# Kernel optimization log

Measured on AMD Instinct MI355X. Metric: run time of the kernel, lower is better.

The kernel has to match this reference:

```python
import math
import jax, jax.numpy as jnp
import numpy as np

H, PQ, PV = 12, 8, 12
C_S = 384
INF, EPS = 1e5, 1e-8
SOFTPLUS_INV_1 = 0.541324854612918


def _rand_rot(key, shape):
    """Random rotation matrices via normalized quaternions, shape + (3,3)."""
    q = jax.random.normal(key, shape + (4,))
    q = q / jnp.linalg.norm(q, axis=-1, keepdims=True)
    w, x, y, z = q[..., 0], q[..., 1], q[..., 2], q[..., 3]
    R = jnp.stack([
        1 - 2 * (y * y + z * z), 2 * (x * y - w * z), 2 * (x * z + w * y),
        2 * (x * y + w * z), 1 - 2 * (x * x + z * z), 2 * (y * z - w * x),
        2 * (x * z - w * y), 2 * (y * z + w * x), 1 - 2 * (x * x + y * y),
    ], axis=-1).reshape(shape + (3, 3))
    return R


def setup_inputs() -> dict:
    key = jax.random.key(0)
    ks = jax.random.split(key, 12)
    B, N1, N2 = 2, 2048, 512
    s1 = jax.random.normal(ks[0], (B, N1, C_S), dtype=jnp.float32)
    s2 = jax.random.normal(ks[1], (B, N2, C_S), dtype=jnp.float32)
    r1_rot = _rand_rot(ks[2], (B, N1)).astype(jnp.float32)
    r2_rot = _rand_rot(ks[3], (B, N2)).astype(jnp.float32)
    r1_trans = jax.random.normal(ks[4], (B, N1, 3), dtype=jnp.float32)
    r2_trans = jax.random.normal(ks[5], (B, N2, 3), dtype=jnp.float32)
    mask1 = jnp.ones((B, N1), dtype=jnp.float32)
    mask2 = jnp.ones((B, N2), dtype=jnp.float32)
    Wq = jax.random.normal(ks[6], (C_S, H * PQ * 3), dtype=jnp.float32) / math.sqrt(C_S)
    Wkv = jax.random.normal(ks[7], (C_S, H * (PQ + PV) * 3), dtype=jnp.float32) / math.sqrt(C_S)
    head_weights = jnp.full((H,), SOFTPLUS_INV_1, dtype=jnp.float32)
    Wout = jax.random.normal(ks[8], (H * PV * 4, C_S), dtype=jnp.float32) * 0.02
    bout = jnp.zeros((C_S,), dtype=jnp.float32)
    return {"s1": s1, "s2": s2, "r1_rot": r1_rot, "r1_trans": r1_trans,
            "r2_rot": r2_rot, "r2_trans": r2_trans, "mask1": mask1, "mask2": mask2,
            "Wq": Wq, "Wkv": Wkv, "head_weights": head_weights,
            "Wout": Wout, "bout": bout}


def reference(s1, s2, r1_rot, r1_trans, r2_rot, r2_trans, mask1, mask2,
              Wq, Wkv, head_weights, Wout, bout):
    B, N1, _ = s1.shape
    N2 = s2.shape[1]

    # query points: linear -> [B,N1,3,H,PQ] (torch split/stack layout) -> local [B,N1,H,PQ,3]
    q = jnp.moveaxis((s1 @ Wq).reshape(B, N1, 3, H, PQ), 2, -1)
    # rigid apply: R x + t (global frame)
    q = jnp.einsum('bimn,bihpn->bihpm', r1_rot, q) + r1_trans[:, :, None, None, :]

    kv = jnp.moveaxis((s2 @ Wkv).reshape(B, N2, 3, H, PQ + PV), 2, -1)
    kv = jnp.einsum('bjmn,bjhpn->bjhpm', r2_rot, kv) + r2_trans[:, :, None, None, :]
    k, v = kv[..., :PQ, :], kv[..., PQ:, :]  # [B,N2,H,PQ,3], [B,N2,H,PV,3]

    # sum_p ||q_p - k_p||^2 via norm expansion (avoids [B,N1,N2,H,PQ,3] tensor)
    qn = jnp.sum(q * q, axis=(-1, -2))                     # [B,N1,H]
    kn = jnp.sum(k * k, axis=(-1, -2))                     # [B,N2,H]
    cross = jnp.einsum('bihpc,bjhpc->bijh', q, k)          # [B,N1,N2,H]
    d2 = qn[:, :, None, :] + kn[:, None, :, :] - 2.0 * cross

    hw = jax.nn.softplus(head_weights) * math.sqrt(1.0 / (3 * (PQ * 9.0 / 2)))
    att = jnp.transpose(-0.5 * d2 * hw, (0, 3, 1, 2))      # [B,H,N1,N2]
    bias = INF * (mask1[:, :, None] * mask2[:, None, :] - 1.0)
    a = jax.nn.softmax(att + bias[:, None], axis=-1)

    o = jnp.einsum('bhij,bjhpc->bihpc', a, v)              # [B,N1,H,PV,3]
    # rigid invert_apply: R^T (x - t), back into local frame of residue i
    o_loc = jnp.einsum('bimn,bihpm->bihpn', r1_rot, o - r1_trans[:, :, None, None, :])

    dists = jnp.sqrt(jnp.sum(o_loc * o_loc, axis=-1) + EPS)   # [B,N1,H,PV]
    o_flat = o_loc.reshape(B, N1, H * PV, 3)
    feats = jnp.concatenate([o_flat[..., 0], o_flat[..., 1], o_flat[..., 2],
                             dists.reshape(B, N1, H * PV)], axis=-1)
    return feats @ Wout + bout
```

## Files before the change

kernel.cpp:

```cpp
#include <hip/hip_runtime.h>
#include <math.h>

#define B_ 2
#define N1_ 2048
#define N2_ 512
#define CS_ 384
#define H_ 12
#define PQ_ 8
#define PV_ 12
#define PKV_ 20
#define CQ_ (H_*PQ_*3)
#define CKV_ (H_*PKV_*3)
#define INF_ 100000.0f
#define HW_SCALE_ 0.09622504486493764f
#define LOG2E_ 1.4426950408889634f

typedef __attribute__((ext_vector_type(8))) short bf16x8;
typedef __attribute__((ext_vector_type(4))) float f32x4;

__device__ inline unsigned short f2bf(float x) {
  unsigned u = __float_as_uint(x);
  u += 0x7fffu + ((u >> 16) & 1u);
  return (unsigned short)(u >> 16);
}

__device__ inline bf16x8 cvt8(const float* __restrict__ p) {
  float4 a = *(const float4*)p;
  float4 b = *(const float4*)(p + 4);
  bf16x8 r;
  r[0] = (short)f2bf(a.x); r[1] = (short)f2bf(a.y);
  r[2] = (short)f2bf(a.z); r[3] = (short)f2bf(a.w);
  r[4] = (short)f2bf(b.x); r[5] = (short)f2bf(b.y);
  r[6] = (short)f2bf(b.z); r[7] = (short)f2bf(b.w);
  return r;
}

#define TQ_   108
#define TKV_  276
#define TWO_  216
#define VPAD_ 72
#define KN_   12
#define S1B_  768
#define S2B_  192
#define PREP_GRID_ (TQ_+TKV_+TWO_+VPAD_+KN_+S1B_+S2B_)
__global__ __launch_bounds__(256) void prep_kernel(
    const float* __restrict__ Wq, const float* __restrict__ Wkv,
    const float* __restrict__ Wout,
    const float* __restrict__ s1, const float* __restrict__ s2,
    unsigned short* __restrict__ wqT, unsigned short* __restrict__ wkvT,
    unsigned short* __restrict__ woutT,
    unsigned short* __restrict__ vtb, float* __restrict__ kn,
    unsigned short* __restrict__ s1b, unsigned short* __restrict__ s2b)
{
  __shared__ float lds[32][33];
  int blk = blockIdx.x, t = threadIdx.x;
  int rr0 = t >> 5, cc = t & 31;

  const float* src = nullptr; unsigned short* dst = nullptr;
  int K = 0, N = 0, k0 = 0, n0 = 0;
  if (blk < TQ_) {
    src = Wq; dst = wqT; K = 384; N = CQ_;
    k0 = (blk % 12) * 32; n0 = (blk / 12) * 32;
  } else if (blk < TQ_ + TKV_) {
    int b2 = blk - TQ_;
    src = Wkv; dst = wkvT; K = 384; N = CKV_;
    k0 = (b2 % 12) * 32; n0 = (b2 / 12) * 32;
  } else if (blk < TQ_ + TKV_ + TWO_) {
    int b3 = blk - TQ_ - TKV_;
    src = Wout; dst = woutT; K = 576; N = CS_;
    k0 = (b3 % 18) * 32; n0 = (b3 / 18) * 32;
  } else if (blk < TQ_ + TKV_ + TWO_ + VPAD_) {
    int idx = (blk - TQ_ - TKV_ - TWO_)*256 + t;
    int f = idx * 8;
    int run = f >> 9, off = f & 511;
    int bh = run / 12, cc2 = 36 + run % 12;
    uint4 z = {0u,0u,0u,0u};
    *(uint4*)(vtb + ((size_t)bh*48 + cc2)*512 + off) = z;
    return;
  } else if (blk < TQ_ + TKV_ + TWO_ + VPAD_ + KN_) {
    int idx = (blk - TQ_ - TKV_ - TWO_ - VPAD_)*256 + t;
    float4 z = {0.f,0.f,0.f,0.f};
    *(float4*)(kn + (size_t)idx*4) = z;
    return;
  } else if (blk < TQ_ + TKV_ + TWO_ + VPAD_ + KN_ + S1B_) {
    size_t idx = (size_t)(blk - TQ_ - TKV_ - TWO_ - VPAD_ - KN_)*256 + t;
    *(bf16x8*)(s1b + idx*8) = cvt8(s1 + idx*8);
    return;
  } else {
    size_t idx = (size_t)(blk - TQ_ - TKV_ - TWO_ - VPAD_ - KN_ - S1B_)*256 + t;
    *(bf16x8*)(s2b + idx*8) = cvt8(s2 + idx*8);
    return;
  }

  #pragma unroll
  for (int rr = 0; rr < 4; ++rr) {
    int r = rr0 + rr*8;
    if (n0 + cc < N) lds[r][cc] = src[(size_t)(k0 + r)*N + n0 + cc];
  }
  __syncthreads();
  #pragma unroll
  for (int rr = 0; rr < 4; ++rr) {
    int r = rr0 + rr*8;
    if (n0 + r < N) dst[(size_t)(n0 + r)*K + k0 + cc] = f2bf(lds[cc][r]);
  }
}

__global__ __launch_bounds__(256) void proj_mfma(
    const unsigned short* __restrict__ s1b, const unsigned short* __restrict__ s2b,
    const unsigned short* __restrict__ wqT, const unsigned short* __restrict__ wkvT,
    const float* __restrict__ r1_rot, const float* __restrict__ r1_trans,
    const float* __restrict__ r2_rot, const float* __restrict__ r2_trans,
    unsigned short* __restrict__ qgb, float* __restrict__ qn,
    unsigned short* __restrict__ kgb, unsigned short* __restrict__ vtb,
    float* __restrict__ kn)
{
  int wave = threadIdx.x >> 6, lane = threadIdx.x & 63;
  int col = lane & 15, g = lane >> 4;

  if (blockIdx.x < 384) {
    int wg = blockIdx.x*4 + wave;
    int strip = wg / 6;
    int nt = wg % 6;
    int i0 = strip * 16;

    f32x4 ax = {0.f,0.f,0.f,0.f}, ay = ax, az = ax;
    const unsigned short* arow = s1b + (size_t)(i0 + col)*CS_;
    const unsigned short* bx = wqT + (size_t)((nt     )*16 + col)*CS_;
    const unsigned short* by = wqT + (size_t)((nt +  6)*16 + col)*CS_;
    const unsigned short* bz = wqT + (size_t)((nt + 12)*16 + col)*CS_;
    #pragma unroll
    for (int k = 0; k < CS_; k += 32) {
      bf16x8 a = *(const bf16x8*)(arow + k + g*8);
      ax = __builtin_amdgcn_mfma_f32_16x16x32_bf16(a, *(const bf16x8*)(bx + k + g*8), ax, 0,0,0);
      ay = __builtin_amdgcn_mfma_f32_16x16x32_bf16(a, *(const bf16x8*)(by + k + g*8), ay, 0,0,0);
      az = __builtin_amdgcn_mfma_f32_16x16x32_bf16(a, *(const bf16x8*)(bz + k + g*8), az, 0,0,0);
    }

    int p = nt*16 + col;
    int h = p >> 3, pq = p & 7;
    float qsum[4];
    #pragma unroll
    for (int r = 0; r < 4; ++r) {
      int row = i0 + g*4 + r;
      const float* R  = r1_rot   + (size_t)row*9;
      const float* tr = r1_trans + (size_t)row*3;
      float x = ax[r], y = ay[r], z = az[r];
      float g0 = R[0]*x + R[1]*y + R[2]*z + tr[0];
      float g1 = R[3]*x + R[4]*y + R[5]*z + tr[1];
      float g2 = R[6]*x + R[7]*y + R[8]*z + tr[2];
      int b = row >> 11, i = row & (N1_-1);
      size_t rbase = ((size_t)(b*H_ + h)*N1_ + i)*32;
      qgb[rbase + pq*3]     = f2bf(g0);
      qgb[rbase + pq*3 + 1] = f2bf(g1);
      qgb[rbase + pq*3 + 2] = f2bf(g2);
      if (pq == 7) {
        uint4 z4 = {0u,0u,0u,0u};
        *(uint4*)(qgb + rbase + 24) = z4;
      }
      qsum[r] = g0*g0 + g1*g1 + g2*g2;
    }
    #pragma unroll
    for (int r = 0; r < 4; ++r) {
      qsum[r] += __shfl_xor(qsum[r], 1);
      qsum[r] += __shfl_xor(qsum[r], 2);
      qsum[r] += __shfl_xor(qsum[r], 4);
    }
    if ((col & 7) == 0) {
      int hh = nt*2 + (col >> 3);
      #pragma unroll
      for (int r = 0; r < 4; ++r) {
        int row = i0 + g*4 + r;
        int b = row >> 11, i = row & (N1_-1);
        qn[(size_t)(b*H_ + hh)*N1_ + i] = qsum[r];
      }
    }
  } else {
    int wg = (blockIdx.x - 384)*4 + wave;
    int strip = wg / 15;
    int nt = wg % 15;
    int row0 = strip * 16;

    f32x4 ax = {0.f,0.f,0.f,0.f}, ay = ax, az = ax;
    const unsigned short* arow = s2b + (size_t)(row0 + col)*CS_;
    const unsigned short* bx = wkvT + (size_t)(nt*16       + col)*CS_;
    const unsigned short* by = wkvT + (size_t)(nt*16 + 240 + col)*CS_;
    const unsigned short* bz = wkvT + (size_t)(nt*16 + 480 + col)*CS_;
    #pragma unroll
    for (int k = 0; k < CS_; k += 32) {
      bf16x8 a = *(const bf16x8*)(arow + k + g*8);
      ax = __builtin_amdgcn_mfma_f32_16x16x32_bf16(a, *(const bf16x8*)(bx + k + g*8), ax, 0,0,0);
      ay = __builtin_amdgcn_mfma_f32_16x16x32_bf16(a, *(const bf16x8*)(by + k + g*8), ay, 0,0,0);
      az = __builtin_amdgcn_mfma_f32_16x16x32_bf16(a, *(const bf16x8*)(bz + k + g*8), az, 0,0,0);
    }

    int p = nt*16 + col;
    int h = p / PKV_, pp = p % PKV_;
    #pragma unroll
    for (int r = 0; r < 4; ++r) {
      int row = row0 + g*4 + r;
      const float* R  = r2_rot   + (size_t)row*9;
      const float* tr = r2_trans + (size_t)row*3;
      float x = ax[r], y = ay[r], z = az[r];
      float g0 = R[0]*x + R[1]*y + R[2]*z + tr[0];
      float g1 = R[3]*x + R[4]*y + R[5]*z + tr[1];
      float g2 = R[6]*x + R[7]*y + R[8]*z + tr[2];
      int b = row >> 9, j = row & (N2_-1);
      int bh = b*H_ + h;
      if (pp < PQ_) {
        size_t base = ((size_t)bh*N2_ + j)*32 + pp*3;
        kgb[base]   = f2bf(g0);
        kgb[base+1] = f2bf(g1);
        kgb[base+2] = f2bf(g2);
        if (pp == 0) {
          uint4 z4 = {0u,0u,0u,0u};
          *(uint4*)(kgb + ((size_t)bh*N2_ + j)*32 + 24) = z4;
        }
        atomicAdd(&kn[(size_t)bh*N2_ + j], g0*g0 + g1*g1 + g2*g2);
      } else {
        int comp = (pp - PQ_)*3;
        size_t base = ((size_t)bh*48 + comp)*512 + j;
        vtb[base]        = f2bf(g0);
        vtb[base + 512]  = f2bf(g1);
        vtb[base + 1024] = f2bf(g2);
      }
    }
  }
}

#define RSTRIDE 72
#define OSTRIDE 51
#define WSLOT 3328
#define FSTRIDE 584
__global__ __launch_bounds__(768) void attn_fused(
    const unsigned short* __restrict__ qgb, const float* __restrict__ qn,
    const unsigned short* __restrict__ kgb, const unsigned short* __restrict__ vtb,
    const float* __restrict__ kn, const float* __restrict__ mask1,
    const float* __restrict__ mask2, const float* __restrict__ hwts,
    const float* __restrict__ rot, const float* __restrict__ trans,
    const unsigned short* __restrict__ woutT, const float* __restrict__ bout,
    float* __restrict__ out)
{
  __shared__ __align__(16) unsigned char ovl[12*WSLOT];
  __shared__ __align__(16) unsigned short feats_s[16][FSTRIDE];
  __shared__ float l_s[12][16];

  int wave = threadIdx.x >> 6;
  int lane = threadIdx.x & 63;
  int col = lane & 15, g = lane >> 4;
  int b = blockIdx.x >> 7;
  int it = blockIdx.x & 127;
  int h = wave;
  int bh = b*H_ + h;

  unsigned short* ps = (unsigned short*)(ovl + wave*WSLOT);
  float*          os = (float*)(ovl + wave*WSLOT);

  float hw   = logf(1.0f + __expf(hwts[h])) * HW_SCALE_;
  float hwl  = hw * LOG2E_;
  float mneg = -INF_ * LOG2E_;

  bf16x8 qa = *(const bf16x8*)(qgb + (((size_t)bh*N1_ + it*16 + col)*32 + g*8));

  float ar[4], m1l[4];
  #pragma unroll
  for (int r = 0; r < 4; ++r) {
    int ig = it*16 + g*4 + r;
    ar[r]  = -0.5f*hwl * qn[(size_t)bh*N1_ + ig];
    m1l[r] = mask1[b*N1_ + ig] * (INF_*LOG2E_);
  }

  f32x4 ot[3];
  #pragma unroll
  for (int m = 0; m < 3; ++m) ot[m] = (f32x4){0.f,0.f,0.f,0.f};
  float l[4] = {0.f,0.f,0.f,0.f};

  const unsigned short* kbase = kgb + (size_t)bh*N2_*32;
  const unsigned short* vbase = vtb + (size_t)bh*48*512;
  const float* knp = kn + (size_t)bh*N2_;
  const float* m2p = mask2 + b*N2_;

  for (int jt = 0; jt < 8; ++jt) {
    int j0 = jt*64;
    #pragma unroll
    for (int nt = 0; nt < 4; ++nt) {
      int jg = j0 + nt*16 + col;
      bf16x8 kb = *(const bf16x8*)(kbase + ((size_t)jg*32 + g*8));
      f32x4 dotv = __builtin_amdgcn_mfma_f32_16x16x32_bf16(
          qa, kb, (f32x4){0.f,0.f,0.f,0.f}, 0, 0, 0);
      float bc  = -0.5f*hwl*knp[jg];
      float m2c = m2p[jg];
      #pragma unroll
      for (int r = 0; r < 4; ++r) {
        float logit = fmaf(hwl, dotv[r], fmaf(m1l[r], m2c, mneg) + (ar[r] + bc));
        float w = __builtin_amdgcn_exp2f(logit);
        l[r] += w;
        ps[(g*4 + r)*RSTRIDE + nt*16 + col] = f2bf(w);
      }
    }
    #pragma unroll
    for (int ks = 0; ks < 2; ++ks) {
      bf16x8 pb = *(const bf16x8*)&ps[col*RSTRIDE + ks*32 + g*8];
      #pragma unroll
      for (int mtv = 0; mtv < 3; ++mtv) {
        bf16x8 va = *(const bf16x8*)(vbase +
            ((size_t)(mtv*16 + col))*512 + j0 + ks*32 + g*8);
        ot[mtv] = __builtin_amdgcn_mfma_f32_16x16x32_bf16(va, pb, ot[mtv], 0, 0, 0);
      }
    }
  }

  #pragma unroll
  for (int r = 0; r < 4; ++r) {
    l[r] += __shfl_xor(l[r], 1);
    l[r] += __shfl_xor(l[r], 2);
    l[r] += __shfl_xor(l[r], 4);
    l[r] += __shfl_xor(l[r], 8);
  }
  __builtin_amdgcn_sched_barrier(0);
  if (col == 0) {
    #pragma unroll
    for (int r = 0; r < 4; ++r) l_s[wave][g*4 + r] = l[r];
  }
  #pragma unroll
  for (int mtv = 0; mtv < 3; ++mtv)
    #pragma unroll
    for (int r = 0; r < 4; ++r)
      os[col*OSTRIDE + mtv*16 + g*4 + r] = ot[mtv][r];
  __syncthreads();

  {
    float inv = 1.0f / l_s[wave][col];
    int ig = it*16 + col;
    int row = b*N1_ + ig;
    const float* R  = rot   + (size_t)row*9;
    const float* tr = trans + (size_t)row*3;
    float R00=R[0],R01=R[1],R02=R[2],R10=R[3],R11=R[4],R12=R[5],R20=R[6],R21=R[7],R22=R[8];
    float t0=tr[0], t1=tr[1], t2=tr[2];
    int h12 = h*PV_;
    #pragma unroll
    for (int p = 0; p < 3; ++p) {
      int pt = g*3 + p;
      float ox = os[col*OSTRIDE + pt*3+0]*inv - t0;
      float oy = os[col*OSTRIDE + pt*3+1]*inv - t1;
      float oz = os[col*OSTRIDE + pt*3+2]*inv - t2;
      float lx = R00*ox + R10*oy + R20*oz;
      float ly = R01*ox + R11*oy + R21*oz;
      float lz = R02*ox + R12*oy + R22*oz;
      float dist = sqrtf(lx*lx + ly*ly + lz*lz + 1e-8f);
      feats_s[col][      h12 + pt] = f2bf(lx);
      feats_s[col][144 + h12 + pt] = f2bf(ly);
      feats_s[col][288 + h12 + pt] = f2bf(lz);
      feats_s[col][432 + h12 + pt] = f2bf(dist);
    }
  }
  __syncthreads();

  {
    int n0 = wave * 32;
    f32x4 acc0 = {0.f,0.f,0.f,0.f}, acc1 = acc0;
    const unsigned short* b0 = woutT + (size_t)(n0      + col)*576;
    const unsigned short* b1 = woutT + (size_t)(n0 + 16 + col)*576;
    #pragma unroll 3
    for (int k = 0; k < 576; k += 32) {
      bf16x8 a = *(const bf16x8*)&feats_s[col][k + g*8];
      acc0 = __builtin_amdgcn_mfma_f32_16x16x32_bf16(a, *(const bf16x8*)(b0 + k + g*8), acc0, 0,0,0);
      acc1 = __builtin_amdgcn_mfma_f32_16x16x32_bf16(a, *(const bf16x8*)(b1 + k + g*8), acc1, 0,0,0);
    }
    int rowbase = b*N1_ + it*16;
    float bb0 = bout[n0 + col];
    float bb1 = bout[n0 + 16 + col];
    #pragma unroll
    for (int r = 0; r < 4; ++r) {
      size_t orow = (size_t)(rowbase + g*4 + r)*CS_;
      out[orow + n0 + col]      = acc0[r] + bb0;
      out[orow + n0 + 16 + col] = acc1[r] + bb1;
    }
  }
}

extern "C" void kernel_launch(void* const* d_in, const int* in_sizes, int n_in,
                              void* d_out, int out_size, void* d_ws, size_t ws_size,
                              hipStream_t stream) {
  const float* s1       = (const float*)d_in[0];
  const float* s2       = (const float*)d_in[1];
  const float* r1_rot   = (const float*)d_in[2];
  const float* r1_trans = (const float*)d_in[3];
  const float* r2_rot   = (const float*)d_in[4];
  const float* r2_trans = (const float*)d_in[5];
  const float* mask1    = (const float*)d_in[6];
  const float* mask2    = (const float*)d_in[7];
  const float* Wq       = (const float*)d_in[8];
  const float* Wkv      = (const float*)d_in[9];
  const float* hwts     = (const float*)d_in[10];
  const float* Wout     = (const float*)d_in[11];
  const float* bout     = (const float*)d_in[12];
  float* out = (float*)d_out;

  float* qn = (float*)d_ws;
  float* kn = qn + (size_t)B_*H_*N1_;
  unsigned short* qgb  = (unsigned short*)(kn + (size_t)B_*H_*N2_);
  unsigned short* kgb  = qgb  + (size_t)B_*H_*N1_*32;
  unsigned short* vtb  = kgb  + (size_t)B_*H_*N2_*32;
  unsigned short* wqT  = vtb  + (size_t)B_*H_*48*512;
  unsigned short* wkvT = wqT  + (size_t)CQ_*CS_;
  unsigned short* woutT= wkvT + (size_t)CKV_*CS_;
  unsigned short* s1b  = woutT+ (size_t)CS_*576;
  unsigned short* s2b  = s1b  + (size_t)B_*N1_*CS_;

  prep_kernel<<<PREP_GRID_, 256, 0, stream>>>(
      Wq, Wkv, Wout, s1, s2, wqT, wkvT, woutT, vtb, kn, s1b, s2b);
  proj_mfma<<<624, 256, 0, stream>>>(s1b, s2b, wqT, wkvT, r1_rot, r1_trans,
                                     r2_rot, r2_trans, qgb, qn, kgb, vtb, kn);
  attn_fused<<<B_*(N1_/16), 768, 0, stream>>>(qgb, qn, kgb, vtb, kn, mask1, mask2,
                                              hwts, r1_rot, r1_trans, woutT, bout, out);
}
```

Baseline: 148.6 us.

## Split attention over key halves and projection K-dim across waves with merges

The attention kernel now launches twice as many blocks, each covering half of the N2 keys. Each block writes its partial output and row sums to a global buffer, and the second block of each pair to finish, detected through an atomic counter, merges both halves and runs the epilogue. The projection kernel splits the K reduction across two waves per output tile and merges the two partial sums through LDS. The aim is more parallelism and better CU occupancy, at the cost of extra global traffic, atomics, fences and a doubled epilogue-free block count.

```diff
diff --git a/kernel.cpp b/kernel.cpp
--- a/kernel.cpp
+++ b/kernel.cpp
@@ -42,7 +42,8 @@
 #define KN_   12
 #define S1B_  768
 #define S2B_  192
-#define PREP_GRID_ (TQ_+TKV_+TWO_+VPAD_+KN_+S1B_+S2B_)
+#define CNTB_ 1
+#define PREP_GRID_ (TQ_+TKV_+TWO_+VPAD_+KN_+S1B_+S2B_+CNTB_)
 __global__ __launch_bounds__(256) void prep_kernel(
     const float* __restrict__ Wq, const float* __restrict__ Wkv,
     const float* __restrict__ Wout,
@@ -50,7 +51,8 @@
     unsigned short* __restrict__ wqT, unsigned short* __restrict__ wkvT,
     unsigned short* __restrict__ woutT,
     unsigned short* __restrict__ vtb, float* __restrict__ kn,
-    unsigned short* __restrict__ s1b, unsigned short* __restrict__ s2b)
+    unsigned short* __restrict__ s1b, unsigned short* __restrict__ s2b,
+    unsigned* __restrict__ cnt)
 {
   __shared__ float lds[32][33];
   int blk = blockIdx.x, t = threadIdx.x;
@@ -86,10 +88,13 @@
     size_t idx = (size_t)(blk - TQ_ - TKV_ - TWO_ - VPAD_ - KN_)*256 + t;
     *(bf16x8*)(s1b + idx*8) = cvt8(s1 + idx*8);
     return;
-  } else {
+  } else if (blk < TQ_ + TKV_ + TWO_ + VPAD_ + KN_ + S1B_ + S2B_) {
     size_t idx = (size_t)(blk - TQ_ - TKV_ - TWO_ - VPAD_ - KN_ - S1B_)*256 + t;
     *(bf16x8*)(s2b + idx*8) = cvt8(s2 + idx*8);
     return;
+  } else {
+    if (t < 256) cnt[t] = 0u;
+    return;
   }
 
   #pragma unroll
@@ -105,7 +110,7 @@
   }
 }
 
-__global__ __launch_bounds__(256) void proj_mfma(
+__global__ __launch_bounds__(512) void proj_mfma(
     const unsigned short* __restrict__ s1b, const unsigned short* __restrict__ s2b,
     const unsigned short* __restrict__ wqT, const unsigned short* __restrict__ wkvT,
     const float* __restrict__ r1_rot, const float* __restrict__ r1_trans,
@@ -114,26 +119,45 @@
     unsigned short* __restrict__ kgb, unsigned short* __restrict__ vtb,
     float* __restrict__ kn)
 {
+  __shared__ float merge_s[4][64][13];
   int wave = threadIdx.x >> 6, lane = threadIdx.x & 63;
   int col = lane & 15, g = lane >> 4;
+  int pr = wave >> 1, kh = wave & 1;
+  int k0 = kh * 192;
 
   if (blockIdx.x < 384) {
-    int wg = blockIdx.x*4 + wave;
-    int strip = wg / 6;
-    int nt = wg % 6;
+    int pid = blockIdx.x*4 + pr;
+    int strip = pid / 6;
+    int nt = pid % 6;
     int i0 = strip * 16;
 
     f32x4 ax = {0.f,0.f,0.f,0.f}, ay = ax, az = ax;
-    const unsigned short* arow = s1b + (size_t)(i0 + col)*CS_;
-    const unsigned short* bx = wqT + (size_t)((nt     )*16 + col)*CS_;
-    const unsigned short* by = wqT + (size_t)((nt +  6)*16 + col)*CS_;
-    const unsigned short* bz = wqT + (size_t)((nt + 12)*16 + col)*CS_;
-    #pragma unroll
-    for (int k = 0; k < CS_; k += 32) {
+    const unsigned short* arow = s1b + (size_t)(i0 + col)*CS_ + k0;
+    const unsigned short* bx = wqT + (size_t)((nt     )*16 + col)*CS_ + k0;
+    const unsigned short* by = wqT + (size_t)((nt +  6)*16 + col)*CS_ + k0;
+    const unsigned short* bz = wqT + (size_t)((nt + 12)*16 + col)*CS_ + k0;
+    #pragma unroll
+    for (int k = 0; k < 192; k += 32) {
       bf16x8 a = *(const bf16x8*)(arow + k + g*8);
       ax = __builtin_amdgcn_mfma_f32_16x16x32_bf16(a, *(const bf16x8*)(bx + k + g*8), ax, 0,0,0);
       ay = __builtin_amdgcn_mfma_f32_16x16x32_bf16(a, *(const bf16x8*)(by + k + g*8), ay, 0,0,0);
       az = __builtin_amdgcn_mfma_f32_16x16x32_bf16(a, *(const bf16x8*)(bz + k + g*8), az, 0,0,0);
+    }
+    if (kh) {
+      #pragma unroll
+      for (int r = 0; r < 4; ++r) {
+        merge_s[pr][lane][r]     = ax[r];
+        merge_s[pr][lane][4 + r] = ay[r];
+        merge_s[pr][lane][8 + r] = az[r];
+      }
+    }
+    __syncthreads();
+    if (kh) return;
+    #pragma unroll
+    for (int r = 0; r < 4; ++r) {
+      ax[r] += merge_s[pr][lane][r];
+      ay[r] += merge_s[pr][lane][4 + r];
+      az[r] += merge_s[pr][lane][8 + r];
     }
 
     int p = nt*16 + col;
@@ -175,22 +199,38 @@
       }
     }
   } else {
-    int wg = (blockIdx.x - 384)*4 + wave;
-    int strip = wg / 15;
-    int nt = wg % 15;
+    int pid = (blockIdx.x - 384)*4 + pr;
+    int strip = pid / 15;
+    int nt = pid % 15;
     int row0 = strip * 16;
 
     f32x4 ax = {0.f,0.f,0.f,0.f}, ay = ax, az = ax;
-    const unsigned short* arow = s2b + (size_t)(row0 + col)*CS_;
-    const unsigned short* bx = wkvT + (size_t)(nt*16       + col)*CS_;
-    const unsigned short* by = wkvT + (size_t)(nt*16 + 240 + col)*CS_;
-    const unsigned short* bz = wkvT + (size_t)(nt*16 + 480 + col)*CS_;
-    #pragma unroll
-    for (int k = 0; k < CS_; k += 32) {
+    const unsigned short* arow = s2b + (size_t)(row0 + col)*CS_ + k0;
+    const unsigned short* bx = wkvT + (size_t)(nt*16       + col)*CS_ + k0;
+    const unsigned short* by = wkvT + (size_t)(nt*16 + 240 + col)*CS_ + k0;
+    const unsigned short* bz = wkvT + (size_t)(nt*16 + 480 + col)*CS_ + k0;
+    #pragma unroll
+    for (int k = 0; k < 192; k += 32) {
       bf16x8 a = *(const bf16x8*)(arow + k + g*8);
       ax = __builtin_amdgcn_mfma_f32_16x16x32_bf16(a, *(const bf16x8*)(bx + k + g*8), ax, 0,0,0);
       ay = __builtin_amdgcn_mfma_f32_16x16x32_bf16(a, *(const bf16x8*)(by + k + g*8), ay, 0,0,0);
       az = __builtin_amdgcn_mfma_f32_16x16x32_bf16(a, *(const bf16x8*)(bz + k + g*8), az, 0,0,0);
+    }
+    if (kh) {
+      #pragma unroll
+      for (int r = 0; r < 4; ++r) {
+        merge_s[pr][lane][r]     = ax[r];
+        merge_s[pr][lane][4 + r] = ay[r];
+        merge_s[pr][lane][8 + r] = az[r];
+      }
+    }
+    __syncthreads();
+    if (kh) return;
+    #pragma unroll
+    for (int r = 0; r < 4; ++r) {
+      ax[r] += merge_s[pr][lane][r];
+      ay[r] += merge_s[pr][lane][4 + r];
+      az[r] += merge_s[pr][lane][8 + r];
     }
 
     int p = nt*16 + col;
@@ -231,24 +271,29 @@
 #define OSTRIDE 51
 #define WSLOT 3328
 #define FSTRIDE 584
-__global__ __launch_bounds__(768) void attn_fused(
+#define PHSTRIDE 784
+__global__ __launch_bounds__(768, 6) void attn_fused(
     const unsigned short* __restrict__ qgb, const float* __restrict__ qn,
     const unsigned short* __restrict__ kgb, const unsigned short* __restrict__ vtb,
     const float* __restrict__ kn, const float* __restrict__ mask1,
     const float* __restrict__ mask2, const float* __restrict__ hwts,
     const float* __restrict__ rot, const float* __restrict__ trans,
     const unsigned short* __restrict__ woutT, const float* __restrict__ bout,
+    float* __restrict__ pbuf, unsigned* __restrict__ cnt,
     float* __restrict__ out)
 {
   __shared__ __align__(16) unsigned char ovl[12*WSLOT];
   __shared__ __align__(16) unsigned short feats_s[16][FSTRIDE];
   __shared__ float l_s[12][16];
+  __shared__ int flag_s;
 
   int wave = threadIdx.x >> 6;
   int lane = threadIdx.x & 63;
   int col = lane & 15, g = lane >> 4;
-  int b = blockIdx.x >> 7;
-  int it = blockIdx.x & 127;
+  int bid = blockIdx.x;
+  int b  = bid >> 8;
+  int it = (bid >> 1) & 127;
+  int jh = bid & 1;
   int h = wave;
   int bh = b*H_ + h;
 
@@ -279,7 +324,7 @@
   const float* knp = kn + (size_t)bh*N2_;
   const float* m2p = mask2 + b*N2_;
 
-  for (int jt = 0; jt < 8; ++jt) {
+  for (int jt = jh*4; jt < jh*4 + 4; ++jt) {
     int j0 = jt*64;
     #pragma unroll
     for (int nt = 0; nt < 4; ++nt) {
@@ -316,7 +361,44 @@
     l[r] += __shfl_xor(l[r], 4);
     l[r] += __shfl_xor(l[r], 8);
   }
-  __builtin_amdgcn_sched_barrier(0);
+
+  float* pb_me  = pbuf + ((size_t)bid*12 + wave) * PHSTRIDE;
+  float* pb_sib = pbuf + ((size_t)(bid ^ 1)*12 + wave) * PHSTRIDE;
+  #pragma unroll
+  for (int mtv = 0; mtv < 3; ++mtv)
+    #pragma unroll
+    for (int r = 0; r < 4; ++r)
+      if (mtv < 2 || g == 0)
+        __hip_atomic_store(&pb_me[col*48 + mtv*16 + g*4 + r], ot[mtv][r],
+                           __ATOMIC_RELAXED, __HIP_MEMORY_SCOPE_AGENT);
+  if (col == 0) {
+    #pragma unroll
+    for (int r = 0; r < 4; ++r)
+      __hip_atomic_store(&pb_me[768 + g*4 + r], l[r],
+                         __ATOMIC_RELAXED, __HIP_MEMORY_SCOPE_AGENT);
+  }
+  __syncthreads();
+  if (threadIdx.x == 0) {
+    __threadfence();
+    unsigned old = atomicAdd(&cnt[bid >> 1], 1u);
+    flag_s = (old == 1);
+  }
+  __syncthreads();
+  if (!flag_s) return;
+  __threadfence();
+
+  #pragma unroll
+  for (int mtv = 0; mtv < 3; ++mtv)
+    #pragma unroll
+    for (int r = 0; r < 4; ++r)
+      if (mtv < 2 || g == 0)
+        ot[mtv][r] += __hip_atomic_load(&pb_sib[col*48 + mtv*16 + g*4 + r],
+                                        __ATOMIC_RELAXED, __HIP_MEMORY_SCOPE_AGENT);
+  #pragma unroll
+  for (int r = 0; r < 4; ++r)
+    l[r] += __hip_atomic_load(&pb_sib[768 + g*4 + r],
+                              __ATOMIC_RELAXED, __HIP_MEMORY_SCOPE_AGENT);
+
   if (col == 0) {
     #pragma unroll
     for (int r = 0; r < 4; ++r) l_s[wave][g*4 + r] = l[r];
@@ -406,11 +488,14 @@
   unsigned short* woutT= wkvT + (size_t)CKV_*CS_;
   unsigned short* s1b  = woutT+ (size_t)CS_*576;
   unsigned short* s2b  = s1b  + (size_t)B_*N1_*CS_;
+  float* pbuf = (float*)(s2b + (size_t)B_*N2_*CS_);
+  unsigned* cnt = (unsigned*)(pbuf + (size_t)512*12*PHSTRIDE);
 
   prep_kernel<<<PREP_GRID_, 256, 0, stream>>>(
-      Wq, Wkv, Wout, s1, s2, wqT, wkvT, woutT, vtb, kn, s1b, s2b);
-  proj_mfma<<<624, 256, 0, stream>>>(s1b, s2b, wqT, wkvT, r1_rot, r1_trans,
+      Wq, Wkv, Wout, s1, s2, wqT, wkvT, woutT, vtb, kn, s1b, s2b, cnt);
+  proj_mfma<<<624, 512, 0, stream>>>(s1b, s2b, wqT, wkvT, r1_rot, r1_trans,
                                      r2_rot, r2_trans, qgb, qn, kgb, vtb, kn);
-  attn_fused<<<B_*(N1_/16), 768, 0, stream>>>(qgb, qn, kgb, vtb, kn, mask1, mask2,
-                                              hwts, r1_rot, r1_trans, woutT, bout, out);
+  attn_fused<<<512, 768, 0, stream>>>(qgb, qn, kgb, vtb, kn, mask1, mask2,
+                                      hwts, r1_rot, r1_trans, woutT, bout,
+                                      pbuf, cnt, out);
 }
```

Result: slower. 267.4 us (+79.9%).
